# Kernel optimization log

Hardware: AMD Instinct MI355X
Metric: run time of the kernel (lower is better)

The kernel has to match this reference:

```python
import jax, jax.numpy as jnp
import numpy as np

EPS = 1e-5  # torch LayerNorm default


def _channel_ln(h, g, b):
    # h: (B, C, N); LayerNorm over channel dim C (biased variance)
    m = jnp.mean(h, axis=1, keepdims=True)
    v = jnp.mean((h - m) ** 2, axis=1, keepdims=True)
    return (h - m) * jax.lax.rsqrt(v + EPS) * g[None, :, None] + b[None, :, None]


def setup_inputs() -> dict:
    key = jax.random.key(0)
    ks = jax.random.split(key, 16)
    B, Cin, Cout, N = 8, 64, 128, 4096
    w = lambda i, shape: jax.random.normal(ks[i], shape, jnp.float32) * 0.02
    return {
        "x": jax.random.normal(ks[0], (B, Cin, N), jnp.float32),
        "p": jax.random.normal(ks[1], (B, 3, N), jnp.float32),
        "W_in": w(2, (Cout, Cin)), "b_in": jnp.zeros((Cout,), jnp.float32),
        "W_q": w(3, (Cout, Cout)),
        "W_k": w(4, (Cout, Cout)),
        "W_v": w(5, (Cout, Cout)),
        "W_d1": w(6, (Cout, 3)), "b_d1": jnp.zeros((Cout,), jnp.float32),
        "W_d2": w(7, (Cout, Cout)), "b_d2": jnp.zeros((Cout,), jnp.float32),
        "W_a": w(8, (Cout, Cout)), "b_a": jnp.zeros((Cout,), jnp.float32),
        "g1": jnp.ones((Cout,), jnp.float32), "be1": jnp.zeros((Cout,), jnp.float32),
        "g2": jnp.ones((Cout,), jnp.float32), "be2": jnp.zeros((Cout,), jnp.float32),
        "W_f1": w(9, (4 * Cout, Cout)), "b_f1": jnp.zeros((4 * Cout,), jnp.float32),
        "W_f2": w(10, (Cout, 4 * Cout)), "b_f2": jnp.zeros((Cout,), jnp.float32),
        "knn_k": 16,
    }


def reference(x, p, W_in, b_in, W_q, W_k, W_v, W_d1, b_d1, W_d2, b_d2,
              W_a, b_a, g1, be1, g2, be2, W_f1, b_f1, W_f2, b_f2, knn_k):
    h = jnp.einsum('oc,bcn->bon', W_in, x) + b_in[None, :, None]  # (B,C,N)
    B, C, N = h.shape
    k = min(int(knn_k), max(1, N - 1))

    h_n = _channel_ln(h, g1, be1)

    # knn on coordinates p: negative squared distance, self excluded
    pt = jnp.swapaxes(p, 1, 2)                                    # (B,N,3)
    xx = jnp.sum(pt * pt, axis=-1)                                # (B,N)
    dist = 2.0 * jnp.einsum('bnd,bmd->bnm', pt, pt) - xx[:, :, None] - xx[:, None, :]
    dist = dist - 1e9 * jnp.eye(N, dtype=dist.dtype)[None]
    idx = jax.lax.top_k(dist, k)[1]                               # (B,N,k) int32

    hn_t = jnp.swapaxes(h_n, 1, 2)                                # (B,N,C)
    q_all = hn_t @ W_q.T
    k_all = hn_t @ W_k.T
    v_all = hn_t @ W_v.T

    bi = jnp.arange(B)[:, None, None]
    k_j = k_all[bi, idx]                                          # (B,N,k,C)
    v_j = v_all[bi, idx]                                          # (B,N,k,C)
    p_j = pt[bi, idx]                                             # (B,N,k,3)

    rel = pt[:, :, None, :] - p_j                                 # (B,N,k,3)
    d = jax.nn.relu(rel @ W_d1.T + b_d1) @ W_d2.T + b_d2          # (B,N,k,C)

    logits = (q_all[:, :, None, :] - k_j + d) @ W_a.T + b_a       # (B,N,k,C)
    a = jax.nn.softmax(logits, axis=2)                            # softmax over k neighbors
    y = jnp.sum(a * (v_j + d), axis=2)                            # (B,N,C)

    h = h + jnp.swapaxes(y, 1, 2)
    h2t = jnp.swapaxes(_channel_ln(h, g2, be2), 1, 2)             # (B,N,C)
    f = jax.nn.relu(h2t @ W_f1.T + b_f1) @ W_f2.T + b_f2          # (B,N,C)
    return h + jnp.swapaxes(f, 1, 2)                              # (B,C,N)
```

## Files before the change

### kernel.cpp

```cpp
#include <hip/hip_runtime.h>
#include <stdint.h>


typedef __attribute__((ext_vector_type(8))) short s8;
typedef __attribute__((ext_vector_type(4))) float f4;

#define MFMA16(a,b,c) __builtin_amdgcn_mfma_f32_16x16x32_bf16(a,b,c,0,0,0)

__device__ __forceinline__ float bf2f(unsigned short u){
  unsigned x = ((unsigned)u) << 16; return __builtin_bit_cast(float, x);
}
__device__ __forceinline__ unsigned short f2bf(float f){
  unsigned x = __builtin_bit_cast(unsigned, f);
  x = x + 0x7FFFu + ((x >> 16) & 1u);
  return (unsigned short)(x >> 16);
}

__device__ __forceinline__ void ce32(unsigned &a, unsigned &b){
  unsigned mn = min(a, b), mx = max(a, b);
  a = mn; b = mx;
}
__device__ __forceinline__ void sort16_u32(unsigned v[16]){
  #pragma unroll
  for (int p = 1; p < 16; p <<= 1){
    #pragma unroll
    for (int k = p; k >= 1; k >>= 1){
      #pragma unroll
      for (int j = k % p; j + k < 16; j += 2*k){
        #pragma unroll
        for (int i = 0; i < k; ++i){
          if (i + j + k < 16){
            if (((i+j) / (2*p)) == ((i+j+k) / (2*p))) ce32(v[i+j], v[i+j+k]);
          }
        }
      }
    }
  }
}
__device__ __forceinline__ void bitonic16_u32(unsigned v[16]){
  #pragma unroll
  for (int k = 8; k >= 1; k >>= 1){
    #pragma unroll
    for (int i = 0; i < 16; ++i){
      if ((i & k) == 0) ce32(v[i], v[i | k]);
    }
  }
}
__device__ __forceinline__ void merge16r(unsigned top[16], const unsigned w[16],
                                         unsigned &r17){
  unsigned t[16], m17 = 0xFFFFFFFFu;
  #pragma unroll
  for (int i = 0; i < 16; ++i){
    unsigned a = top[i], b = w[15 - i];
    t[i] = min(a, b);
    m17 = min(m17, max(a, b));
  }
  bitonic16_u32(t);
  #pragma unroll
  for (int i = 0; i < 16; ++i) top[i] = t[i];
  r17 = min(r17, m17);
}
__device__ __forceinline__ void drainP(unsigned* br, int &cnt, unsigned top[16],
                                       unsigned &r17, unsigned &thr){
  unsigned v[16];
  #pragma unroll
  for (int j = 0; j < 16; ++j){
    unsigned t = br[j];
    v[j] = (j < cnt) ? t : 0xFFFFFFFFu;
  }
  cnt = 0;
  sort16_u32(v);
  merge16r(top, v, r17);
  thr = top[15];
}

__global__ __launch_bounds__(128) void k_p1(const float* __restrict__ W_a,
    const float* __restrict__ W_k, const float* __restrict__ W_q, const float* __restrict__ W_d2,
    float* __restrict__ tk, float* __restrict__ tq, float* __restrict__ td){
  int which = blockIdx.x >> 7, row = blockIdx.x & 127, c = threadIdx.x;
  const float* X = (which == 0) ? W_k : ((which == 1) ? W_q : W_d2);
  float* O = (which == 0) ? tk : ((which == 1) ? tq : td);
  float acc = 0.f;
  #pragma unroll 8
  for (int i = 0; i < 128; ++i) acc += W_a[row*128 + i] * X[i*128 + c];
  O[row*128 + c] = acc;
}

__global__ __launch_bounds__(256) void k_pack(
    const float* __restrict__ p, const float* __restrict__ W_v,
    const float* __restrict__ W_d1, const float* __restrict__ b_d1,
    const float* __restrict__ W_in, const float* __restrict__ W_f1, const float* __restrict__ W_f2,
    const float* __restrict__ W_a, const float* __restrict__ b_a, const float* __restrict__ b_d2,
    const float* __restrict__ W_d2,
    const float* __restrict__ tk, const float* __restrict__ tq, const float* __restrict__ td,
    float4* __restrict__ pp, unsigned short* __restrict__ wcatf, unsigned short* __restrict__ wf1f,
    unsigned short* __restrict__ wf2f, unsigned short* __restrict__ wd2f,
    unsigned short* __restrict__ wdaf, unsigned short* __restrict__ w1f,
    unsigned short* __restrict__ winf, float* __restrict__ ball){
  int id0 = blockIdx.x * blockDim.x + threadIdx.x;
  int stride = gridDim.x * blockDim.x;
  for (int i = id0; i < 32768; i += stride){
    int b = i >> 12, m = i & 4095;
    float xx = p[(b*3 + 0)*4096 + m];
    float yy = p[(b*3 + 1)*4096 + m];
    float zz = p[(b*3 + 2)*4096 + m];
    pp[i] = float4{xx, yy, zz, xx*xx + yy*yy + zz*zz};
  }
  for (int i = id0; i < 49152; i += stride){
    int tg = i >> 11, s = (i >> 9) & 3, l = (i >> 3) & 63, j = i & 7;
    int row = tg*16 + (l & 15), k = s*32 + (l >> 4)*8 + j;
    float v;
    if (row < 128) v = tk[row*128 + k];
    else if (row < 256) v = W_v[(row - 128)*128 + k];
    else v = tq[(row - 256)*128 + k];
    wcatf[i] = f2bf(v);
  }
  for (int i = id0; i < 65536; i += stride){
    int tg = i >> 11, s = (i >> 9) & 3, l = (i >> 3) & 63, j = i & 7;
    int row = tg*16 + (l & 15), k = s*32 + (l >> 4)*8 + j;
    wf1f[i] = f2bf(W_f1[row*128 + k]);
  }
  for (int i = id0; i < 65536; i += stride){
    int mt = i >> 13, s = (i >> 9) & 15, l = (i >> 3) & 63, j = i & 7;
    int row = mt*16 + (l & 15), k = s*32 + (l >> 4)*8 + j;
    wf2f[i] = f2bf(W_f2[row*512 + k]);
  }
  for (int i = id0; i < 16384; i += stride){
    int tg = i >> 11, s = (i >> 9) & 3, l = (i >> 3) & 63, j = i & 7;
    int row = tg*16 + (l & 15), k = s*32 + (l >> 4)*8 + j;
    wd2f[i] = f2bf(W_d2[row*128 + k]);
  }
  for (int i = id0; i < 16384; i += stride){
    int tg = i >> 11, s = (i >> 9) & 3, l = (i >> 3) & 63, j = i & 7;
    int row = tg*16 + (l & 15), k = s*32 + (l >> 4)*8 + j;
    wdaf[i] = f2bf(td[row*128 + k]);
  }
  for (int i = id0; i < 4096; i += stride){
    int tg = i >> 9, l = (i >> 3) & 63, j = i & 7;
    int c = tg*16 + (l & 15);
    float v = 0.f;
    if (l < 16 && j < 4) v = (j < 3) ? W_d1[c*3 + j] : b_d1[c];
    w1f[i] = f2bf(v);
  }
  for (int i = id0; i < 8192; i += stride){
    int tg = i >> 10, s = (i >> 9) & 1, l = (i >> 3) & 63, j = i & 7;
    int row = tg*16 + (l & 15), k = s*32 + (l >> 4)*8 + j;
    winf[i] = f2bf(W_in[row*64 + k]);
  }
  for (int o = id0; o < 128; o += stride){
    float acc = b_a[o];
    for (int c = 0; c < 128; ++c) acc += W_a[o*128 + c] * b_d2[c];
    ball[o] = acc;
  }
}

__global__ __launch_bounds__(256) void k_a(const float* __restrict__ x,
    const unsigned short* __restrict__ WINF, const float* __restrict__ b_in,
    const float* __restrict__ g1, const float* __restrict__ be1,
    float* __restrict__ H, unsigned short* __restrict__ HN){
  __shared__ unsigned short xT[64][72];
  int tid = threadIdx.x;
  int bb = blockIdx.x >> 6;
  int n0 = (blockIdx.x & 63) * 64;
  for (int i = tid; i < 4096; i += 256){
    int c = i >> 6, nn = i & 63;
    xT[nn][c] = f2bf(x[((size_t)(bb*64 + c))*4096 + n0 + nn]);
  }
  __syncthreads();
  int lane = tid & 63, w = tid >> 6, m16 = lane & 15, g = lane >> 4;
  const char* xb = (const char*)&xT[0][0];
  s8 a0 = *(const s8*)(xb + (w*16 + m16)*144 + 16*g);
  s8 a1 = *(const s8*)(xb + (w*16 + m16)*144 + 64 + 16*g);
  const f4 zf = {0.f, 0.f, 0.f, 0.f};
  f4 acc[8];
  #pragma unroll
  for (int t = 0; t < 8; ++t) acc[t] = zf;
  #pragma unroll
  for (int t = 0; t < 8; ++t){
    s8 b0 = *(const s8*)(WINF + ((size_t)(t*2 + 0)*64 + lane)*8);
    s8 b1 = *(const s8*)(WINF + ((size_t)(t*2 + 1)*64 + lane)*8);
    acc[t] = MFMA16(a0, b0, acc[t]);
    acc[t] = MFMA16(a1, b1, acc[t]);
  }
  float mean[4], rstd[4];
  #pragma unroll
  for (int r = 0; r < 4; ++r){
    float ls = 0.f, lq = 0.f;
    #pragma unroll
    for (int t = 0; t < 8; ++t){
      float v = acc[t][r] + b_in[t*16 + m16];
      ls += v; lq += v*v;
    }
    ls += __shfl_xor(ls, 1); ls += __shfl_xor(ls, 2); ls += __shfl_xor(ls, 4); ls += __shfl_xor(ls, 8);
    lq += __shfl_xor(lq, 1); lq += __shfl_xor(lq, 2); lq += __shfl_xor(lq, 4); lq += __shfl_xor(lq, 8);
    float mn = ls * (1.f/128.f);
    float vr = lq * (1.f/128.f) - mn*mn;
    mean[r] = mn;
    rstd[r] = rsqrtf(vr + 1e-5f);
  }
  int ptbase = blockIdx.x*64 + w*16;
  #pragma unroll
  for (int t = 0; t < 8; ++t){
    int o = t*16 + m16;
    float bi = b_in[o], gg = g1[o], be = be1[o];
    #pragma unroll
    for (int r = 0; r < 4; ++r){
      int pt = ptbase + 4*g + r;
      float v = acc[t][r] + bi;
      H[(size_t)pt*128 + o] = v;
      HN[(size_t)pt*128 + o] = f2bf((v - mean[r])*rstd[r]*gg + be);
    }
  }
}

template<int MODE>
__global__ __launch_bounds__(256) void k_gemm(const unsigned short* __restrict__ A,
    const unsigned short* __restrict__ Btab, const float* __restrict__ bias,
    unsigned short* __restrict__ out){
  int lane = threadIdx.x & 63, w = threadIdx.x >> 6;
  int m0 = blockIdx.x*64 + w*16;
  int by = blockIdx.y;
  int m16 = lane & 15, g = lane >> 4;
  const f4 zf = {0.f, 0.f, 0.f, 0.f};
  f4 acc[8];
  #pragma unroll
  for (int t = 0; t < 8; ++t) acc[t] = zf;
  #pragma unroll
  for (int s = 0; s < 4; ++s){
    s8 af = *(const s8*)(A + ((size_t)(m0 + m16))*128 + s*32 + g*8);
    #pragma unroll
    for (int t = 0; t < 8; ++t){
      s8 bf = *(const s8*)(Btab + ((size_t)((by*8 + t)*4 + s)*64 + lane)*8);
      acc[t] = MFMA16(af, bf, acc[t]);
    }
  }
  #pragma unroll
  for (int t = 0; t < 8; ++t){
    int col = by*128 + t*16 + m16;
    #pragma unroll
    for (int r = 0; r < 4; ++r){
      int pt = m0 + 4*g + r;
      float v = acc[t][r];
      if (MODE == 0){
        int pos = (col < 128) ? 2*col : ((col < 256) ? 2*(col - 128) + 1 : col);
        out[(size_t)pt*384 + pos] = f2bf(v);
      } else {
        v = fmaxf(v + bias[col], 0.f);
        out[(size_t)pt*512 + col] = f2bf(v);
      }
    }
  }
}

__global__ __launch_bounds__(256) void k_f2(const unsigned short* __restrict__ wf2f,
    const unsigned short* __restrict__ Z, const float* __restrict__ b_f2,
    float* __restrict__ out){
  int lane = threadIdx.x & 63, w = threadIdx.x >> 6;
  int mt = blockIdx.x*4 + w;
  int p0 = blockIdx.y*128;
  int m16 = lane & 15, g = lane >> 4;
  const f4 zf = {0.f, 0.f, 0.f, 0.f};
  f4 acc[8];
  #pragma unroll
  for (int t = 0; t < 8; ++t) acc[t] = zf;
  #pragma unroll 4
  for (int s = 0; s < 16; ++s){
    s8 af = *(const s8*)(wf2f + ((size_t)(mt*16 + s)*64 + lane)*8);
    #pragma unroll
    for (int t = 0; t < 8; ++t){
      s8 bf = *(const s8*)(Z + (size_t)(p0 + t*16 + m16)*512 + s*32 + g*8);
      acc[t] = MFMA16(af, bf, acc[t]);
    }
  }
  #pragma unroll
  for (int t = 0; t < 8; ++t){
    #pragma unroll
    for (int r = 0; r < 4; ++r){
      int o = mt*16 + 4*g + r;
      int pt = p0 + t*16 + m16;
      int b = pt >> 12, n = pt & 4095;
      size_t ix = (((size_t)(b*128 + o)) << 12) | (unsigned)n;
      out[ix] += acc[t][r] + b_f2[o];
    }
  }
}

__global__ __launch_bounds__(256, 6) void k_knn(const float4* __restrict__ PP,
    int* __restrict__ IDXo){
  __shared__ __align__(16) char smem[17920];
  int tid = threadIdx.x;
  int b = blockIdx.x >> 7;
  int tile = blockIdx.x & 127;
  int q = tid & 31;
  int sub = tid >> 5;
  int qn = tile*32 + q;
  const float4* pb = PP + (size_t)b*4096;
  float4 me = pb[qn];
  int base = sub << 9;

  unsigned* br32 = (unsigned*)(smem + tid*68);

  unsigned top32[16];
  #pragma unroll
  for (int j = 0; j < 16; ++j) top32[j] = 0xFFFFFFFFu;
  unsigned r17 = 0xFFFFFFFFu;
  unsigned thr = 0xFFFFFFFFu;
  int cnt = 0;
  float4 c0 = pb[base+0], c1 = pb[base+1], c2 = pb[base+2], c3 = pb[base+3];
  #pragma unroll 1
  for (int ii = 0; ii < 128; ++ii){
    float4 d0 = c0, d1 = c1, d2v = c2, d3 = c3;
    int nb = base + (((ii + 1) & 127) << 2);
    c0 = pb[nb+0]; c1 = pb[nb+1]; c2 = pb[nb+2]; c3 = pb[nb+3];
    int m0 = base + ii*4;
    {
      float dx = me.x-d0.x, dy = me.y-d0.y, dz = me.z-d0.z;
      unsigned key = (__builtin_bit_cast(unsigned, dx*dx+dy*dy+dz*dz) & 0xFFFFF000u) | (unsigned)m0;
      if (m0 != qn){ if (key < thr){ br32[cnt] = key; ++cnt; } else r17 = min(r17, key); }
    }
    {
      float dx = me.x-d1.x, dy = me.y-d1.y, dz = me.z-d1.z;
      unsigned key = (__builtin_bit_cast(unsigned, dx*dx+dy*dy+dz*dz) & 0xFFFFF000u) | (unsigned)(m0+1);
      if (m0+1 != qn){ if (key < thr){ br32[cnt] = key; ++cnt; } else r17 = min(r17, key); }
    }
    {
      float dx = me.x-d2v.x, dy = me.y-d2v.y, dz = me.z-d2v.z;
      unsigned key = (__builtin_bit_cast(unsigned, dx*dx+dy*dy+dz*dz) & 0xFFFFF000u) | (unsigned)(m0+2);
      if (m0+2 != qn){ if (key < thr){ br32[cnt] = key; ++cnt; } else r17 = min(r17, key); }
    }
    {
      float dx = me.x-d3.x, dy = me.y-d3.y, dz = me.z-d3.z;
      unsigned key = (__builtin_bit_cast(unsigned, dx*dx+dy*dy+dz*dz) & 0xFFFFF000u) | (unsigned)(m0+3);
      if (m0+3 != qn){ if (key < thr){ br32[cnt] = key; ++cnt; } else r17 = min(r17, key); }
    }
    if (__any(cnt >= 13)) drainP(br32, cnt, top32, r17, thr);
  }
  drainP(br32, cnt, top32, r17, thr);

  unsigned* pub = (unsigned*)smem;
  #pragma unroll
  for (int step = 4; step >= 1; step >>= 1){
    __syncthreads();
    if (sub >= step && sub < 2*step){
      unsigned* row = pub + (size_t)((sub - step)*32 + q)*17;
      #pragma unroll
      for (int j = 0; j < 16; ++j) row[j] = top32[j];
      row[16] = r17;
    }
    __syncthreads();
    if (sub < step){
      unsigned other[16];
      unsigned* row = pub + (size_t)(sub*32 + q)*17;
      #pragma unroll
      for (int j = 0; j < 16; ++j) other[j] = row[j];
      r17 = min(r17, row[16]);
      merge16r(top32, other, r17);
    }
  }

  unsigned key16 = top32[15];
  bool flag = false;
  if (sub == 0){
    flag = ((r17 >> 12) - (key16 >> 12)) <= 1u;
    if (!flag){
      int* op = IDXo + ((size_t)(b*4096 + qn))*16;
      #pragma unroll
      for (int j = 0; j < 16; ++j) op[j] = (int)(top32[j] & 0xFFFu);
    }
  }

  if ((tid >> 6) == 0){
    int lane = tid & 63;
    unsigned long long flags = __ballot(flag);
    int* pcnt = (int*)(smem + 17408);
    unsigned* pool = (unsigned*)(smem + 17412);
    while (flags){
      int L = __ffsll((long long)flags) - 1;
      flags &= flags - 1;
      int qf = tile*32 + L;
      float qx = __shfl(me.x, L), qy = __shfl(me.y, L), qz = __shfl(me.z, L);
      unsigned k16 = __shfl(key16, L);
      unsigned t16 = k16 >> 12;
      unsigned bhi = (t16 >= 0xFFFFDu) ? 0xFFFFFFFFu : ((t16 + 2) << 12);
      if (lane == 0) atomicExch(pcnt, 0);
      #pragma unroll 4
      for (int it = 0; it < 64; ++it){
        int m = it*64 + lane;
        float4 cd = pb[m];
        float dx = qx-cd.x, dy = qy-cd.y, dz = qz-cd.z;
        unsigned bits = __builtin_bit_cast(unsigned, dx*dx+dy*dy+dz*dz);
        if (m != qf && bits < bhi){
          int s = atomicAdd(pcnt, 1);
          if (s < 64) pool[s] = (unsigned)m;
        }
      }
      int pn = atomicAdd(pcnt, 0);
      if (pn > 64) pn = 64;
      unsigned long long kk = ~0ull;
      if (lane < pn){
        int m = pool[lane];
        float4 cd = pb[m];
        double ddx = (double)qx - (double)cd.x;
        double ddy = (double)qy - (double)cd.y;
        double ddz = (double)qz - (double)cd.z;
        double d2 = ddx*ddx + ddy*ddy + ddz*ddz;
        kk = (__builtin_bit_cast(unsigned long long, d2) & ~0xFFFull) | (unsigned)m;
      }
      #pragma unroll
      for (int k2 = 2; k2 <= 64; k2 <<= 1){
        #pragma unroll
        for (int j = k2 >> 1; j >= 1; j >>= 1){
          unsigned long long o = __shfl_xor(kk, j);
          bool up = ((lane & k2) == 0);
          bool keepmin = (((lane & j) == 0) == up);
          unsigned long long mn = kk < o ? kk : o;
          unsigned long long mx = kk < o ? o : kk;
          kk = keepmin ? mn : mx;
        }
      }
      if (lane < 16)
        IDXo[((size_t)(b*4096 + qf))*16 + lane] = (int)(unsigned)(kk & 0xFFFull);
    }
  }
}

__global__ __launch_bounds__(256) void k_attn(const float* __restrict__ pcoord,
    const int* __restrict__ IDX, const unsigned short* __restrict__ QKV,
    const unsigned short* __restrict__ W1F, const unsigned short* __restrict__ WD2F,
    const unsigned short* __restrict__ WDAF, const float* __restrict__ b_d2,
    const float* __restrict__ BALL, unsigned short* __restrict__ Y){
  __shared__ unsigned short kv_sh[4][4][16][64];
  __shared__ unsigned short t1_sh[4][2048];
  __shared__ int idx_sh[4][4][16];
  int tid = threadIdx.x;
  int w = tid >> 6, lane = tid & 63;
  int m16 = lane & 15, g = lane >> 4;
  int P0 = blockIdx.x*16 + w*4;
  const f4 zf = {0.f, 0.f, 0.f, 0.f};
  if (lane < 16){
    #pragma unroll
    for (int q = 0; q < 4; ++q) idx_sh[w][q][lane] = IDX[(size_t)(P0 + q)*16 + lane];
  }
  s8 a[4][4];
  #pragma unroll
  for (int q = 0; q < 4; ++q){
    int pt = P0 + q;
    int bq = pt >> 12, nn = pt & 4095;
    const float* pb = pcoord + (size_t)bq*3*4096;
    s8 arel = {0,0,0,0,0,0,0,0};
    if (lane < 16){
      int jn = idx_sh[w][q][m16];
      float rx = pb[nn] - pb[jn];
      float ry = pb[4096 + nn] - pb[4096 + jn];
      float rz = pb[8192 + nn] - pb[8192 + jn];
      arel[0] = (short)f2bf(rx); arel[1] = (short)f2bf(ry);
      arel[2] = (short)f2bf(rz); arel[3] = (short)0x3F80;
    }
    f4 t1a[8];
    #pragma unroll
    for (int t = 0; t < 8; ++t){
      s8 bw = *(const s8*)(W1F + ((size_t)t*64 + lane)*8);
      t1a[t] = MFMA16(arel, bw, zf);
    }
    #pragma unroll
    for (int t = 0; t < 8; ++t){
      int c = t*16 + m16;
      #pragma unroll
      for (int r = 0; r < 4; ++r){
        int m = 4*g + r;
        int byt = (m*256 + c*2) ^ ((m & 7) << 4);
        t1_sh[w][byt >> 1] = f2bf(fmaxf(t1a[t][r], 0.f));
      }
    }
    const char* t1b = (const char*)&t1_sh[w][0];
    #pragma unroll
    for (int s = 0; s < 4; ++s){
      int byt = (m16*256 + 64*s + 16*g) ^ ((m16 & 7) << 4);
      a[q][s] = *(const s8*)(t1b + byt);
    }
  }
  #pragma unroll 1
  for (int pass = 0; pass < 4; ++pass){
    uint4 gk[4][2];
    #pragma unroll
    for (int q = 0; q < 4; ++q){
      int pt = P0 + q, bq = pt >> 12;
      #pragma unroll
      for (int i2 = 0; i2 < 2; ++i2){
        int mm = i2*8 + (lane >> 3);
        int jn = idx_sh[w][q][mm];
        gk[q][i2] = *(const uint4*)((const char*)QKV
            + ((size_t)(bq*4096 + jn))*768 + pass*128 + (lane & 7)*16);
      }
    }
    #pragma unroll
    for (int q = 0; q < 4; ++q){
      #pragma unroll
      for (int i2 = 0; i2 < 2; ++i2)
        *(uint4*)((char*)&kv_sh[w][q][i2*8][0] + lane*16) = gk[q][i2];
    }
    #pragma unroll
    for (int tl = 0; tl < 2; ++tl){
      int tg = pass*2 + tl;
      f4 dacc[4], lacc[4];
      #pragma unroll
      for (int q = 0; q < 4; ++q){ dacc[q] = zf; lacc[q] = zf; }
      #pragma unroll
      for (int s = 0; s < 4; ++s){
        s8 wd2 = *(const s8*)(WD2F + ((size_t)(tg*4 + s)*64 + lane)*8);
        s8 wda = *(const s8*)(WDAF + ((size_t)(tg*4 + s)*64 + lane)*8);
        #pragma unroll
        for (int q = 0; q < 4; ++q){
          dacc[q] = MFMA16(a[q][s], wd2, dacc[q]);
          lacc[q] = MFMA16(a[q][s], wda, lacc[q]);
        }
      }
      int col = tg*16 + m16;
      float bd2c = b_d2[col];
      float ballc = BALL[col];
      #pragma unroll
      for (int q = 0; q < 4; ++q){
        int pt = P0 + q;
        float qac = bf2f(QKV[(size_t)pt*384 + 256 + col]);
        float lg[4], dd[4], vv[4];
        #pragma unroll
        for (int r = 0; r < 4; ++r){
          int m = 4*g + r;
          unsigned kvp = *(const unsigned*)&kv_sh[w][q][m][(tl*16 + m16)*2];
          float ka = bf2f((unsigned short)(kvp & 0xFFFFu));
          vv[r] = bf2f((unsigned short)(kvp >> 16));
          lg[r] = lacc[q][r] + qac - ka + ballc;
          dd[r] = dacc[q][r] + bd2c;
        }
        float mx = fmaxf(fmaxf(lg[0], lg[1]), fmaxf(lg[2], lg[3]));
        mx = fmaxf(mx, __shfl_xor(mx, 16));
        mx = fmaxf(mx, __shfl_xor(mx, 32));
        float e0 = __expf(lg[0] - mx), e1 = __expf(lg[1] - mx);
        float e2 = __expf(lg[2] - mx), e3 = __expf(lg[3] - mx);
        float ss = e0 + e1 + e2 + e3;
        ss += __shfl_xor(ss, 16); ss += __shfl_xor(ss, 32);
        float inv = 1.f / ss;
        float yp = e0*(vv[0] + dd[0]) + e1*(vv[1] + dd[1])
                 + e2*(vv[2] + dd[2]) + e3*(vv[3] + dd[3]);
        yp *= inv;
        yp += __shfl_xor(yp, 16); yp += __shfl_xor(yp, 32);
        if (lane < 16) Y[(size_t)pt*128 + col] = f2bf(yp);
      }
    }
  }
}

__global__ __launch_bounds__(256) void k_d1(const float* __restrict__ H,
    const unsigned short* __restrict__ Y, const float* __restrict__ g2,
    const float* __restrict__ be2, float* __restrict__ outp,
    unsigned short* __restrict__ HN2){
  __shared__ float tile[128*65];
  int tid = threadIdx.x;
  int w = tid >> 6, lane = tid & 63;
  int pt16 = lane & 15, g = lane >> 4;
  int n64 = w*16 + pt16;
  int ptbase = blockIdx.x * 64;
  int pt = ptbase + n64;
  int c0 = g*32;
  const float4* h4 = (const float4*)(H + (size_t)pt*128 + c0);
  const uint4*  y4 = (const uint4*)((const char*)Y + (size_t)pt*256 + (size_t)c0*2);
  float h2[32];
  float ls = 0.f, lq = 0.f;
  #pragma unroll
  for (int i = 0; i < 4; ++i){
    float4 ha = h4[2*i], hb = h4[2*i + 1];
    uint4 yv = y4[i];
    float v0 = ha.x + bf2f((unsigned short)(yv.x & 0xFFFFu));
    float v1 = ha.y + bf2f((unsigned short)(yv.x >> 16));
    float v2 = ha.z + bf2f((unsigned short)(yv.y & 0xFFFFu));
    float v3 = ha.w + bf2f((unsigned short)(yv.y >> 16));
    float v4 = hb.x + bf2f((unsigned short)(yv.z & 0xFFFFu));
    float v5 = hb.y + bf2f((unsigned short)(yv.z >> 16));
    float v6 = hb.z + bf2f((unsigned short)(yv.w & 0xFFFFu));
    float v7 = hb.w + bf2f((unsigned short)(yv.w >> 16));
    h2[8*i+0]=v0; h2[8*i+1]=v1; h2[8*i+2]=v2; h2[8*i+3]=v3;
    h2[8*i+4]=v4; h2[8*i+5]=v5; h2[8*i+6]=v6; h2[8*i+7]=v7;
    ls += v0+v1+v2+v3+v4+v5+v6+v7;
    lq += v0*v0+v1*v1+v2*v2+v3*v3+v4*v4+v5*v5+v6*v6+v7*v7;
  }
  ls += __shfl_xor(ls, 16); ls += __shfl_xor(ls, 32);
  lq += __shfl_xor(lq, 16); lq += __shfl_xor(lq, 32);
  float mn = ls * (1.f/128.f);
  float vr = lq * (1.f/128.f) - mn*mn;
  float rs = rsqrtf(vr + 1e-5f);
  const float4* g4  = (const float4*)(g2 + c0);
  const float4* be4 = (const float4*)(be2 + c0);
  #pragma unroll
  for (int i = 0; i < 4; ++i){
    float4 ga = g4[2*i], gb = g4[2*i+1], ba = be4[2*i], bb2 = be4[2*i+1];
    unsigned uu[4];
    uu[0] = (unsigned)f2bf((h2[8*i+0]-mn)*rs*ga.x + ba.x)
          | ((unsigned)f2bf((h2[8*i+1]-mn)*rs*ga.y + ba.y) << 16);
    uu[1] = (unsigned)f2bf((h2[8*i+2]-mn)*rs*ga.z + ba.z)
          | ((unsigned)f2bf((h2[8*i+3]-mn)*rs*ga.w + ba.w) << 16);
    uu[2] = (unsigned)f2bf((h2[8*i+4]-mn)*rs*gb.x + bb2.x)
          | ((unsigned)f2bf((h2[8*i+5]-mn)*rs*gb.y + bb2.y) << 16);
    uu[3] = (unsigned)f2bf((h2[8*i+6]-mn)*rs*gb.z + bb2.z)
          | ((unsigned)f2bf((h2[8*i+7]-mn)*rs*gb.w + bb2.w) << 16);
    *(uint4*)((char*)HN2 + (size_t)pt*256 + (size_t)c0*2 + i*16)
        = make_uint4(uu[0], uu[1], uu[2], uu[3]);
  }
  int swz = g << 4;
  #pragma unroll
  for (int k = 0; k < 32; ++k)
    tile[(c0 + k)*65 + (n64 ^ swz)] = h2[k];
  __syncthreads();
  int bb = ptbase >> 12;
  int nb = ptbase & 4095;
  #pragma unroll 8
  for (int k = 0; k < 32; ++k){
    int c = w*32 + k;
    float v = tile[c*65 + (lane ^ ((((unsigned)c >> 5) & 3) << 4))];
    outp[(((size_t)(bb*128 + c)) << 12) | (unsigned)(nb + lane)] = v;
  }
}

extern "C" void kernel_launch(void* const* d_in, const int* in_sizes, int n_in,
                              void* d_out, int out_size, void* d_ws, size_t ws_size,
                              hipStream_t stream){
  const float* x    = (const float*)d_in[0];
  const float* p    = (const float*)d_in[1];
  const float* W_in = (const float*)d_in[2];
  const float* b_in = (const float*)d_in[3];
  const float* W_q  = (const float*)d_in[4];
  const float* W_k  = (const float*)d_in[5];
  const float* W_v  = (const float*)d_in[6];
  const float* W_d1 = (const float*)d_in[7];
  const float* b_d1 = (const float*)d_in[8];
  const float* W_d2 = (const float*)d_in[9];
  const float* b_d2 = (const float*)d_in[10];
  const float* W_a  = (const float*)d_in[11];
  const float* b_a  = (const float*)d_in[12];
  const float* g1   = (const float*)d_in[13];
  const float* be1  = (const float*)d_in[14];
  const float* g2   = (const float*)d_in[15];
  const float* be2  = (const float*)d_in[16];
  const float* W_f1 = (const float*)d_in[17];
  const float* b_f1 = (const float*)d_in[18];
  const float* W_f2 = (const float*)d_in[19];
  const float* b_f2 = (const float*)d_in[20];
  float* out = (float*)d_out;
  char* ws = (char*)d_ws;

  float*          H    = (float*)(ws + 0);
  unsigned short* HN   = (unsigned short*)(ws + 16777216);
  unsigned short* QKV  = (unsigned short*)(ws + 25165824);
  unsigned short* Z    = (unsigned short*)(ws + 16777216);
  unsigned short* Y    = (unsigned short*)(ws + 50331648);
  unsigned short* HN2  = (unsigned short*)(ws + 58720256);
  int*            IDX  = (int*)(ws + 67108864);
  float4*         PP   = (float4*)(ws + 69206016);
  char* tab = ws + 69730304;
  unsigned short* WCATF = (unsigned short*)(tab + 0);
  unsigned short* WF1F  = (unsigned short*)(tab + 98304);
  unsigned short* WF2F  = (unsigned short*)(tab + 229376);
  unsigned short* WD2F  = (unsigned short*)(tab + 360448);
  unsigned short* WDAF  = (unsigned short*)(tab + 393216);
  unsigned short* W1F   = (unsigned short*)(tab + 425984);
  unsigned short* WINF  = (unsigned short*)(tab + 434176);
  float*          BALL  = (float*)(tab + 450560);
  float*          TK    = (float*)(tab + 451072);
  float*          TQ    = (float*)(tab + 516608);
  float*          TD    = (float*)(tab + 582144);

  k_p1<<<dim3(384), dim3(128), 0, stream>>>(W_a, W_k, W_q, W_d2, TK, TQ, TD);
  k_pack<<<dim3(256), dim3(256), 0, stream>>>(p, W_v, W_d1, b_d1, W_in, W_f1, W_f2,
      W_a, b_a, b_d2, W_d2, TK, TQ, TD,
      PP, WCATF, WF1F, WF2F, WD2F, WDAF, W1F, WINF, BALL);
  k_knn<<<dim3(1024), dim3(256), 0, stream>>>(PP, IDX);
  k_a<<<dim3(512), dim3(256), 0, stream>>>(x, WINF, b_in, g1, be1, H, HN);
  k_gemm<0><<<dim3(512, 3), dim3(256), 0, stream>>>(HN, WCATF, nullptr, QKV);
  k_attn<<<dim3(2048), dim3(256), 0, stream>>>(p, IDX, QKV, W1F, WD2F, WDAF, b_d2, BALL, Y);
  k_d1<<<dim3(512), dim3(256), 0, stream>>>(H, Y, g2, be2, out, HN2);
  k_gemm<1><<<dim3(512, 4), dim3(256), 0, stream>>>(HN2, WF1F, b_f1, Z);
  k_f2<<<dim3(2, 256), dim3(256), 0, stream>>>(WF2F, Z, b_f2, out);
}
```

Measured before the change: 395.1 us.

## Prefetch next-pass neighbor K/V gathers and pad shared layout in attention kernel

The attention kernel now issues the global gathers of neighbor K/V rows and query values for the next pass before computing the current pass, so gather latency overlaps the MFMA and softmax work. The per-wave shared buffer is merged into one padded region (row stride 144 bytes) to reduce LDS bank conflicts, and query values are loaded once per pass and broadcast with shuffles instead of per-column global loads. Occupancy hints are raised for both the kNN and attention kernels. Holding the prefetched values in registers increases register pressure, which may conflict with the new occupancy targets.

```diff
diff --git a/kernel.cpp b/kernel.cpp
--- a/kernel.cpp
+++ b/kernel.cpp
@@ -285,7 +285,7 @@
   }
 }
 
-__global__ __launch_bounds__(256, 6) void k_knn(const float4* __restrict__ PP,
+__global__ __launch_bounds__(256, 8) void k_knn(const float4* __restrict__ PP,
     int* __restrict__ IDXo){
   __shared__ __align__(16) char smem[17920];
   int tid = threadIdx.x;
@@ -424,23 +424,24 @@
   }
 }
 
-__global__ __launch_bounds__(256) void k_attn(const float* __restrict__ pcoord,
+__global__ __launch_bounds__(256, 4) void k_attn(const float* __restrict__ pcoord,
     const int* __restrict__ IDX, const unsigned short* __restrict__ QKV,
     const unsigned short* __restrict__ W1F, const unsigned short* __restrict__ WD2F,
     const unsigned short* __restrict__ WDAF, const float* __restrict__ b_d2,
     const float* __restrict__ BALL, unsigned short* __restrict__ Y){
-  __shared__ unsigned short kv_sh[4][4][16][64];
-  __shared__ unsigned short t1_sh[4][2048];
+  __shared__ __align__(16) char smem[36864];
   __shared__ int idx_sh[4][4][16];
   int tid = threadIdx.x;
   int w = tid >> 6, lane = tid & 63;
   int m16 = lane & 15, g = lane >> 4;
   int P0 = blockIdx.x*16 + w*4;
+  char* wbase = smem + w*9216;
   const f4 zf = {0.f, 0.f, 0.f, 0.f};
   if (lane < 16){
     #pragma unroll
     for (int q = 0; q < 4; ++q) idx_sh[w][q][lane] = IDX[(size_t)(P0 + q)*16 + lane];
   }
+  unsigned short* t1s = (unsigned short*)wbase;
   s8 a[4][4];
   #pragma unroll
   for (int q = 0; q < 4; ++q){
@@ -469,35 +470,55 @@
       for (int r = 0; r < 4; ++r){
         int m = 4*g + r;
         int byt = (m*256 + c*2) ^ ((m & 7) << 4);
-        t1_sh[w][byt >> 1] = f2bf(fmaxf(t1a[t][r], 0.f));
-      }
-    }
-    const char* t1b = (const char*)&t1_sh[w][0];
+        t1s[byt >> 1] = f2bf(fmaxf(t1a[t][r], 0.f));
+      }
+    }
+    const char* t1b = (const char*)t1s;
     #pragma unroll
     for (int s = 0; s < 4; ++s){
       int byt = (m16*256 + 64*s + 16*g) ^ ((m16 & 7) << 4);
       a[q][s] = *(const s8*)(t1b + byt);
     }
   }
+  asm volatile("s_waitcnt lgkmcnt(0)" ::: "memory");
+  __builtin_amdgcn_sched_barrier(0);
+
+  uint4 gk[4][2];
+  float qav[4];
+  #pragma unroll
+  for (int q = 0; q < 4; ++q){
+    int pt = P0 + q, bq = pt >> 12;
+    #pragma unroll
+    for (int i2 = 0; i2 < 2; ++i2){
+      int mm = i2*8 + (lane >> 3);
+      int jn = idx_sh[w][q][mm];
+      gk[q][i2] = *(const uint4*)((const char*)QKV
+          + ((size_t)(bq*4096 + jn))*768 + (lane & 7)*16);
+    }
+    qav[q] = bf2f(QKV[(size_t)pt*384 + 256 + (lane & 31)]);
+  }
   #pragma unroll 1
   for (int pass = 0; pass < 4; ++pass){
-    uint4 gk[4][2];
     #pragma unroll
     for (int q = 0; q < 4; ++q){
-      int pt = P0 + q, bq = pt >> 12;
-      #pragma unroll
-      for (int i2 = 0; i2 < 2; ++i2){
-        int mm = i2*8 + (lane >> 3);
-        int jn = idx_sh[w][q][mm];
-        gk[q][i2] = *(const uint4*)((const char*)QKV
-            + ((size_t)(bq*4096 + jn))*768 + pass*128 + (lane & 7)*16);
-      }
-    }
-    #pragma unroll
-    for (int q = 0; q < 4; ++q){
       #pragma unroll
       for (int i2 = 0; i2 < 2; ++i2)
-        *(uint4*)((char*)&kv_sh[w][q][i2*8][0] + lane*16) = gk[q][i2];
+        *(uint4*)(wbase + q*2304 + (i2*8 + (lane >> 3))*144 + (lane & 7)*16) = gk[q][i2];
+    }
+    float qv[4] = {qav[0], qav[1], qav[2], qav[3]};
+    if (pass < 3){
+      #pragma unroll
+      for (int q = 0; q < 4; ++q){
+        int pt = P0 + q, bq = pt >> 12;
+        #pragma unroll
+        for (int i2 = 0; i2 < 2; ++i2){
+          int mm = i2*8 + (lane >> 3);
+          int jn = idx_sh[w][q][mm];
+          gk[q][i2] = *(const uint4*)((const char*)QKV
+              + ((size_t)(bq*4096 + jn))*768 + (pass + 1)*128 + (lane & 7)*16);
+        }
+        qav[q] = bf2f(QKV[(size_t)pt*384 + 256 + (pass + 1)*32 + (lane & 31)]);
+      }
     }
     #pragma unroll
     for (int tl = 0; tl < 2; ++tl){
@@ -521,15 +542,15 @@
       #pragma unroll
       for (int q = 0; q < 4; ++q){
         int pt = P0 + q;
-        float qac = bf2f(QKV[(size_t)pt*384 + 256 + col]);
+        float qbase = __shfl(qv[q], tl*16 + m16) + ballc;
         float lg[4], dd[4], vv[4];
         #pragma unroll
         for (int r = 0; r < 4; ++r){
           int m = 4*g + r;
-          unsigned kvp = *(const unsigned*)&kv_sh[w][q][m][(tl*16 + m16)*2];
+          unsigned kvp = *(const unsigned*)(wbase + q*2304 + m*144 + (tl*16 + m16)*4);
           float ka = bf2f((unsigned short)(kvp & 0xFFFFu));
           vv[r] = bf2f((unsigned short)(kvp >> 16));
-          lg[r] = lacc[q][r] + qac - ka + ballc;
+          lg[r] = lacc[q][r] + qbase - ka;
           dd[r] = dacc[q][r] + bd2c;
         }
         float mx = fmaxf(fmaxf(lg[0], lg[1]), fmaxf(lg[2], lg[3]));
```

New measurement: 479.7 us. +21.4%, slower.
